# Optimization experiments

Hardware: AMD Instinct MI355X
Metric: run time of the kernel (lower is better)

## Reference

```python
import jax, jax.numpy as jnp
import numpy as np
from jax import lax

EPS = 1e-5
KH, KW, PAD, DIL = 3, 3, 1, 1


def _bilinear_gather(x, py, px):
    """x: [B,C,H,W]; py/px: [B,K,H,W] float sample coords. Returns [B,C,K,H,W].
    Zero-padding semantics (torchvision deform_conv2d): corners outside the image contribute 0."""
    B, C, H, W = x.shape
    K = py.shape[1]
    y0 = jnp.floor(py)
    x0 = jnp.floor(px)
    wy1 = py - y0
    wy0 = 1.0 - wy1
    wx1 = px - x0
    wx0 = 1.0 - wx1
    xf = x.reshape(B, C, H * W)

    def corner(yc, xc, w):
        valid = (yc >= 0) & (yc <= H - 1) & (xc >= 0) & (xc <= W - 1)
        yi = jnp.clip(yc, 0, H - 1).astype(jnp.int32)
        xi = jnp.clip(xc, 0, W - 1).astype(jnp.int32)
        lin = (yi * W + xi).reshape(B, -1)  # [B, K*H*W]
        v = jax.vmap(lambda xb, lb: xb[:, lb])(xf, lin)  # [B, C, K*H*W]
        return v * (w * valid.astype(x.dtype)).reshape(B, 1, -1)

    out = (corner(y0, x0, wy0 * wx0)
           + corner(y0, x0 + 1.0, wy0 * wx1)
           + corner(y0 + 1.0, x0, wy1 * wx0)
           + corner(y0 + 1.0, x0 + 1.0, wy1 * wx1))
    return out.reshape(B, C, K, H, W)


def _deform_conv(x, offset, w):
    B, C, H, W = x.shape
    K = KH * KW
    off = offset.reshape(B, K, 2, H, W)  # (dy, dx) per kernel tap
    ki = (jnp.arange(K) // KW - PAD).astype(x.dtype)  # kernel row offset (dil=1)
    kj = (jnp.arange(K) % KW - PAD).astype(x.dtype)
    hh = jnp.arange(H).astype(x.dtype)
    ww = jnp.arange(W).astype(x.dtype)
    py = hh[None, None, :, None] + ki[None, :, None, None] + off[:, :, 0]
    px = ww[None, None, None, :] + kj[None, :, None, None] + off[:, :, 1]
    val = _bilinear_gather(x, py, px)  # [B,C,K,H,W]
    return jnp.einsum('bckhw,ock->bohw', val, w.reshape(w.shape[0], C, K))


def _bn(x, gamma, beta, mean, var):
    inv = gamma * lax.rsqrt(var + EPS)
    return x * inv[None, :, None, None] + (beta - mean * inv)[None, :, None, None]


def setup_inputs() -> dict:
    key = jax.random.key(0)
    ks = jax.random.split(key, 12)
    B, C, H, W = 4, 128, 128, 128
    return {
        'x': jax.random.normal(ks[0], (B, C, H, W), jnp.float32),
        'offset': jax.random.normal(ks[1], (B, 2 * KH * KW, H, W), jnp.float32),
        'w1': jax.random.normal(ks[2], (C, C, KH, KW), jnp.float32) * 0.05,
        'bn1_gamma': jax.random.uniform(ks[3], (C,), jnp.float32, 0.5, 1.5),
        'bn1_beta': jax.random.normal(ks[4], (C,), jnp.float32) * 0.1,
        'bn1_mean': jax.random.normal(ks[5], (C,), jnp.float32) * 0.1,
        'bn1_var': jax.random.uniform(ks[6], (C,), jnp.float32, 0.5, 1.5),
        'w2': jax.random.normal(ks[7], (C, C, KH, KW), jnp.float32) * 0.05,
        'bn2_gamma': jax.random.uniform(ks[8], (C,), jnp.float32, 0.5, 1.5),
        'bn2_beta': jax.random.normal(ks[9], (C,), jnp.float32) * 0.1,
        'bn2_mean': jax.random.normal(ks[10], (C,), jnp.float32) * 0.1,
        'bn2_var': jax.random.uniform(ks[11], (C,), jnp.float32, 0.5, 1.5),
    }


def reference(x, offset, w1, bn1_gamma, bn1_beta, bn1_mean, bn1_var,
              w2, bn2_gamma, bn2_beta, bn2_mean, bn2_var):
    identity = x
    out = _deform_conv(x, offset, w1)
    out = jax.nn.relu(_bn(out, bn1_gamma, bn1_beta, bn1_mean, bn1_var))
    out = lax.conv_general_dilated(out, w2, window_strides=(1, 1),
                                   padding=((PAD, PAD), (PAD, PAD)),
                                   dimension_numbers=('NCHW', 'OIHW', 'NCHW'))
    out = _bn(out, bn2_gamma, bn2_beta, bn2_mean, bn2_var)
    out = jax.nn.relu(out + identity)
    return out
```

## Files before the change

kernel.cpp:

```cpp
#include <hip/hip_runtime.h>
#include <hip/hip_fp16.h>
#include <stdint.h>

#define B_ 4
#define C_ 128
#define H_ 128
#define W_ 128
#define HW 16384

typedef _Float16 h8 __attribute__((ext_vector_type(8)));
typedef float f32x16 __attribute__((ext_vector_type(16)));

__device__ __forceinline__ unsigned cvtpk_f16(float lo, float hi) {
    auto r = __builtin_amdgcn_cvt_pkrtz(lo, hi);
    return *(unsigned*)&r;
}

__device__ __forceinline__ unsigned blend_h2(unsigned c0, unsigned c1, unsigned c2, unsigned c3,
                                             __half2 G0, __half2 G1, __half2 G2, __half2 G3) {
    __half2 s = __hmul2(G0, *(__half2*)&c0);
    s = __hfma2(G1, *(__half2*)&c1, s);
    s = __hfma2(G2, *(__half2*)&c2, s);
    s = __hfma2(G3, *(__half2*)&c3, s);
    return *(unsigned*)&s;
}

__device__ __forceinline__ void gll16(const void* g, void* l) {
    __builtin_amdgcn_global_load_lds((const unsigned int*)g, (unsigned int*)l, 16, 0, 0);
}

__global__ __launch_bounds__(256) void prep_all(const float* __restrict__ x,
                                                unsigned short* __restrict__ xh,
                                                const float* __restrict__ w1,
                                                const float* __restrict__ w2,
                                                unsigned short* __restrict__ w1f,
                                                unsigned short* __restrict__ w2t,
                                                unsigned short* __restrict__ o1p,
                                                const float* g1, const float* b1, const float* m1, const float* v1,
                                                const float* g2, const float* b2, const float* m2, const float* v2,
                                                float* inv1, float* sh1, float* inv2, float* sh2) {
    __shared__ unsigned short tile[32][36];
    int blk = blockIdx.x;
    int tid = threadIdx.x;
    if (blk >= 1282) {
        int nb = blk - 1282;
        int wt = nb & 3, ct = (nb >> 2) & 3, h = (nb >> 4) & 127, b = nb >> 11;
        int c = tid >> 3, seg = tid & 7;
        const float* srcp = x + ((size_t)((b * 128 + ct * 32 + c) * 128 + h) * 128) + wt * 32 + seg * 4;
        float4 v = *(const float4*)srcp;
        uint2 pk;
        pk.x = cvtpk_f16(v.x, v.y);
        pk.y = cvtpk_f16(v.z, v.w);
        *(uint2*)&tile[c][seg * 4] = pk;
        __syncthreads();
        int w = tid >> 3, s2 = tid & 7;
        unsigned a0 = tile[s2 * 4 + 0][w];
        unsigned a1 = tile[s2 * 4 + 1][w];
        unsigned a2 = tile[s2 * 4 + 2][w];
        unsigned a3 = tile[s2 * 4 + 3][w];
        uint2 o;
        o.x = (a1 << 16) | a0;
        o.y = (a3 << 16) | a2;
        *(uint2*)(xh + ((size_t)((b * 128 + h) * 128 + wt * 32 + w) * 128) + ct * 32 + s2 * 4) = o;
        return;
    }
    if (blk < 1152) {
        int i = blk * 256 + tid;
        if (i < 147456) {
            int o = i / 1152, rem = i % 1152;
            int c = rem / 9, tap = rem % 9;
            _Float16 hv = (_Float16)w1[i];
            int s = o >> 5;
            int ks = c >> 4;
            int l = (o & 31) | (((c >> 3) & 1) << 5);
            int jj = c & 7;
            w1f[(((tap * 4 + s) * 8 + ks) * 64 + l) * 8 + jj] = *(unsigned short*)&hv;
        } else {
            int j = i - 147456;
            int o = j / 1152, rem = j % 1152;
            int c = rem / 9, tap = rem % 9;
            _Float16 hv = (_Float16)w2[j];
            w2t[o * 1152 + tap * 128 + c] = *(unsigned short*)&hv;
        }
    } else if (blk < 1281) {
        int i = (blk - 1152) * 256 + tid;
        if (i < 33024) {
            int chunk = i & 15;
            int pos = i >> 4;
            int b = pos / 516;
            int r = pos % 516;
            int row, col;
            if (r < 130)      { row = 0;   col = r; }
            else if (r < 260) { row = 129; col = r - 130; }
            else { int j = r - 260; row = 1 + (j >> 1); col = (j & 1) * 129; }
            uint4 z = {0u, 0u, 0u, 0u};
            *(uint4*)((char*)o1p + (size_t)((b * 130 + row) * 130 + col) * 256 + chunk * 16) = z;
        }
    } else {
        if (tid < 128) {
            float iv = g1[tid] * rsqrtf(v1[tid] + 1e-5f);
            inv1[tid] = iv; sh1[tid] = b1[tid] - m1[tid] * iv;
        } else {
            int u = tid - 128;
            float iv = g2[u] * rsqrtf(v2[u] + 1e-5f);
            inv2[u] = iv; sh2[u] = b2[u] - m2[u] * iv;
        }
    }
}

__global__ __launch_bounds__(512, 4) void gemm1_k(
    const unsigned short* __restrict__ xh,
    const float* __restrict__ off,
    const unsigned short* __restrict__ w1f,
    const float* __restrict__ inv1,
    const float* __restrict__ sh1,
    unsigned short* __restrict__ out1p) {
    __shared__ __align__(16) char ldsv[2][16384];

    int bid = blockIdx.x;
    int swz = ((bid & 7) << 7) | (bid >> 3);
    int half = swz & 1, h = (swz >> 1) & 127, b = swz >> 8;
    int w0 = half * 64;
    int tid = threadIdx.x;
    int bH = b * H_;
    const char* xb8 = (const char*)xh;

    if (tid < 256) {
        int prow = tid >> 4;
        int seg = tid & 15;
        int sb = seg * 16;

        float dy[4], dx[4];
        unsigned PX[4][4];
        float g[4][4];
        uint4 buf[2][4];

#define OFFLOAD(TT) do { \
    int dyB_ = ((b * 18 + 2 * (TT)) * H_ + h) * W_ + w0; \
    _Pragma("unroll") \
    for (int c_ = 0; c_ < 4; ++c_) { \
        int p_ = prow + c_ * 16; \
        dy[c_] = off[dyB_ + p_]; \
        dx[c_] = off[dyB_ + HW + p_]; \
    } \
} while (0)

#define COORD(TT) do { \
    int kh_ = (TT) / 3 - 1, kw_ = (TT) % 3 - 1; \
    _Pragma("unroll") \
    for (int c_ = 0; c_ < 4; ++c_) { \
        int p_ = prow + c_ * 16; \
        float py_ = (float)(h + kh_) + dy[c_]; \
        float px_ = (float)(w0 + p_ + kw_) + dx[c_]; \
        float y0f_ = floorf(py_), x0f_ = floorf(px_); \
        int y0_ = (int)y0f_, x0_ = (int)x0f_; \
        float wy1_ = py_ - y0f_, wx1_ = px_ - x0f_; \
        float wy0_ = 1.f - wy1_, wx0_ = 1.f - wx1_; \
        int y1_ = y0_ + 1, x1_ = x0_ + 1; \
        g[c_][0] = ((unsigned)y0_ < 128u && (unsigned)x0_ < 128u) ? wy0_ * wx0_ : 0.f; \
        g[c_][1] = ((unsigned)y0_ < 128u && (unsigned)x1_ < 128u) ? wy0_ * wx1_ : 0.f; \
        g[c_][2] = ((unsigned)y1_ < 128u && (unsigned)x0_ < 128u) ? wy1_ * wx0_ : 0.f; \
        g[c_][3] = ((unsigned)y1_ < 128u && (unsigned)x1_ < 128u) ? wy1_ * wx1_ : 0.f; \
        int y0c_ = min(max(y0_, 0), 127), y1c_ = min(max(y1_, 0), 127); \
        int x0c_ = min(max(x0_, 0), 127), x1c_ = min(max(x1_, 0), 127); \
        int r0_ = (bH + y0c_) * W_, r1_ = (bH + y1c_) * W_; \
        PX[c_][0] = (unsigned)((r0_ + x0c_) * 256) + sb; \
        PX[c_][1] = (unsigned)((r0_ + x1c_) * 256) + sb; \
        PX[c_][2] = (unsigned)((r1_ + x0c_) * 256) + sb; \
        PX[c_][3] = (unsigned)((r1_ + x1c_) * 256) + sb; \
    } \
} while (0)

#define ISSUE2(cA, cB) do { \
    _Pragma("unroll") \
    for (int k_ = 0; k_ < 4; ++k_) buf[0][k_] = *(const uint4*)(xb8 + PX[cA][k_]); \
    _Pragma("unroll") \
    for (int k_ = 0; k_ < 4; ++k_) buf[1][k_] = *(const uint4*)(xb8 + PX[cB][k_]); \
} while (0)

#define BLEND1(VP, CC, BI) do { \
    __half2 G0_ = __float2half2_rn(g[CC][0]); \
    __half2 G1_ = __float2half2_rn(g[CC][1]); \
    __half2 G2_ = __float2half2_rn(g[CC][2]); \
    __half2 G3_ = __float2half2_rn(g[CC][3]); \
    uint4 st_; \
    st_.x = blend_h2(buf[BI][0].x, buf[BI][1].x, buf[BI][2].x, buf[BI][3].x, G0_, G1_, G2_, G3_); \
    st_.y = blend_h2(buf[BI][0].y, buf[BI][1].y, buf[BI][2].y, buf[BI][3].y, G0_, G1_, G2_, G3_); \
    st_.z = blend_h2(buf[BI][0].z, buf[BI][1].z, buf[BI][2].z, buf[BI][3].z, G0_, G1_, G2_, G3_); \
    st_.w = blend_h2(buf[BI][0].w, buf[BI][1].w, buf[BI][2].w, buf[BI][3].w, G0_, G1_, G2_, G3_); \
    int row_ = prow + (CC) * 16; \
    *(uint4*)(&ldsv[VP][0] + row_ * 256 + ((seg ^ (row_ & 15)) << 4)) = st_; \
} while (0)

#define GATHER(VP) do { \
    ISSUE2(0, 1); \
    BLEND1(VP, 0, 0); BLEND1(VP, 1, 1); \
    ISSUE2(2, 3); \
    BLEND1(VP, 2, 0); BLEND1(VP, 3, 1); \
} while (0)

        OFFLOAD(0);
        COORD(0);
        GATHER(0);
        OFFLOAD(1);
        __syncthreads();
        for (int t = 0; t < 9; ++t) {
            if (t < 8) {
                COORD(t + 1);
                GATHER((t + 1) & 1);
                if (t < 7) OFFLOAD(t + 2);
            }
            __syncthreads();
        }
#undef OFFLOAD
#undef COORD
#undef ISSUE2
#undef BLEND1
#undef GATHER
    } else {
        int ctid = tid - 256;
        int lane = ctid & 63, wq = ctid >> 6;
        int lp = lane & 31, hi = lane >> 5;
        int lsw = lp & 15;
        int bRow0 = lp * 256;
        int bRow1 = (32 + lp) * 256;

        f32x16 acc0 = {};
        f32x16 acc1 = {};
        h8 wreg[2][8];

        {
            const unsigned short* wb = w1f + wq * 4096 + lane * 8;
            #pragma unroll
            for (int ks = 0; ks < 8; ++ks) wreg[0][ks] = *(const h8*)(wb + ks * 512);
        }
        __syncthreads();
        #pragma unroll
        for (int t = 0; t < 9; ++t) {
            if (t < 8) {
                const unsigned short* wb = w1f + ((t + 1) * 4 + wq) * 4096 + lane * 8;
                #pragma unroll
                for (int ks = 0; ks < 8; ++ks) wreg[(t + 1) & 1][ks] = *(const h8*)(wb + ks * 512);
            }
            const char* vcur = &ldsv[t & 1][0];
            #pragma unroll
            for (int ks = 0; ks < 8; ++ks) {
                int q0 = 2 * ks + hi;
                int sl = (q0 ^ lsw) << 4;
                h8 b0 = *(const h8*)(vcur + bRow0 + sl);
                h8 b1 = *(const h8*)(vcur + bRow1 + sl);
                h8 a = wreg[t & 1][ks];
                acc0 = __builtin_amdgcn_mfma_f32_32x32x16_f16(a, b0, acc0, 0, 0, 0);
                acc1 = __builtin_amdgcn_mfma_f32_32x32x16_f16(a, b1, acc1, 0, 0, 0);
            }
            __syncthreads();
        }

        #pragma unroll
        for (int j = 0; j < 2; ++j) {
            int p = w0 + j * 32 + lp;
            size_t rowbase = (size_t)((b * 130 + h + 1) * 130 + 1 + p) * 128;
            #pragma unroll
            for (int k = 0; k < 4; ++k) {
                int o0 = wq * 32 + k * 8 + hi * 4;
                float4 iv = *(const float4*)(inv1 + o0);
                float4 sv = *(const float4*)(sh1 + o0);
                float e0, e1, e2, e3;
                if (j == 0) {
                    e0 = acc0[4 * k + 0]; e1 = acc0[4 * k + 1];
                    e2 = acc0[4 * k + 2]; e3 = acc0[4 * k + 3];
                } else {
                    e0 = acc1[4 * k + 0]; e1 = acc1[4 * k + 1];
                    e2 = acc1[4 * k + 2]; e3 = acc1[4 * k + 3];
                }
                float v0 = fmaxf(fmaf(e0, iv.x, sv.x), 0.f);
                float v1 = fmaxf(fmaf(e1, iv.y, sv.y), 0.f);
                float v2 = fmaxf(fmaf(e2, iv.z, sv.z), 0.f);
                float v3 = fmaxf(fmaf(e3, iv.w, sv.w), 0.f);
                uint2 pk2;
                pk2.x = cvtpk_f16(v0, v1);
                pk2.y = cvtpk_f16(v2, v3);
                *(uint2*)(out1p + rowbase + o0) = pk2;
            }
        }
    }
}

__global__ __launch_bounds__(512, 4) void gemm2_k(
    const unsigned short* __restrict__ out1p,
    const unsigned short* __restrict__ w2t,
    const unsigned short* __restrict__ xh,
    const float* __restrict__ inv2,
    const float* __restrict__ sh2,
    float* __restrict__ outp) {
    __shared__ __align__(16) char ldsS[33280];
    __shared__ __align__(16) char ldsw[32768];

    int bid = blockIdx.x;
    int swz = ((bid & 7) << 6) | (bid >> 3);
    int h = swz & 127, b = swz >> 7;
    int tid = threadIdx.x, lane = tid & 63, wv = tid >> 6;
    int wo = wv >> 2, wp = wv & 3;
    int lp = lane & 31, hi = lane >> 5;

    f32x16 acc0 = {};
    f32x16 acc1 = {};

    int aRow0 = (wo * 64 + lp) * 256;
    int aRow1 = aRow0 + 32 * 256;
    int lsw = lp & 15;

    for (int kh = 0; kh < 3; ++kh) {
        __syncthreads();
        const char* srow = (const char*)out1p + (size_t)((b * 130 + h + kh) * 130) * 256;
        #pragma unroll
        for (int it = 0; it < 5; ++it) {
            int ci = it * 512 + tid;
            if (ci < 2080) {
                int r = ci >> 4, q = ci & 15;
                gll16(srow + r * 256 + ((q ^ (r & 15)) << 4), ldsS + ci * 16);
            }
        }
        for (int kw = 0; kw < 3; ++kw) {
            if (kw) __syncthreads();
            int tap = kh * 3 + kw;
            #pragma unroll
            for (int it = 0; it < 4; ++it) {
                int ci = it * 512 + tid;
                int o = ci >> 4, q = ci & 15;
                gll16((const char*)w2t + o * 2304 + tap * 256 + ((q ^ (o & 15)) << 4), ldsw + ci * 16);
            }
            __syncthreads();
            int pr = (wp * 32 + lp + kw) * 256;
            int prw = (wp * 32 + lp + kw) & 15;
            #pragma unroll
            for (int ks = 0; ks < 8; ++ks) {
                int q0 = 2 * ks + hi;
                h8 bb = *(const h8*)(ldsS + pr + ((q0 ^ prw) << 4));
                int sl = (q0 ^ lsw) << 4;
                h8 a0 = *(const h8*)(ldsw + aRow0 + sl);
                h8 a1 = *(const h8*)(ldsw + aRow1 + sl);
                acc0 = __builtin_amdgcn_mfma_f32_32x32x16_f16(a0, bb, acc0, 0, 0, 0);
                acc1 = __builtin_amdgcn_mfma_f32_32x32x16_f16(a1, bb, acc1, 0, 0, 0);
            }
        }
    }

    int p = wp * 32 + lp;
    const unsigned short* xrow = xh + (size_t)((b * 128 + h) * 128 + p) * 128;
    #pragma unroll
    for (int t = 0; t < 2; ++t) {
        #pragma unroll
        for (int k = 0; k < 4; ++k) {
            int o0 = wo * 64 + t * 32 + k * 8 + hi * 4;
            uint2 rx = *(const uint2*)(xrow + o0);
            __half2 hx0 = *(__half2*)&rx.x;
            __half2 hx1 = *(__half2*)&rx.y;
            float x0 = __low2float(hx0), x1 = __high2float(hx0);
            float x2 = __low2float(hx1), x3 = __high2float(hx1);
            float e0, e1, e2, e3;
            if (t == 0) {
                e0 = acc0[4 * k + 0]; e1 = acc0[4 * k + 1];
                e2 = acc0[4 * k + 2]; e3 = acc0[4 * k + 3];
            } else {
                e0 = acc1[4 * k + 0]; e1 = acc1[4 * k + 1];
                e2 = acc1[4 * k + 2]; e3 = acc1[4 * k + 3];
            }
            size_t idx = ((size_t)(b * C_ + o0) * H_ + h) * W_ + p;
            outp[idx]            = fmaxf(fmaf(e0, inv2[o0 + 0], sh2[o0 + 0]) + x0, 0.f);
            outp[idx + HW]       = fmaxf(fmaf(e1, inv2[o0 + 1], sh2[o0 + 1]) + x1, 0.f);
            outp[idx + 2 * HW]   = fmaxf(fmaf(e2, inv2[o0 + 2], sh2[o0 + 2]) + x2, 0.f);
            outp[idx + 3 * HW]   = fmaxf(fmaf(e3, inv2[o0 + 3], sh2[o0 + 3]) + x3, 0.f);
        }
    }
}

extern "C" void kernel_launch(void* const* d_in, const int* in_sizes, int n_in,
                              void* d_out, int out_size, void* d_ws, size_t ws_size,
                              hipStream_t stream) {
    const float* x   = (const float*)d_in[0];
    const float* off = (const float*)d_in[1];
    const float* w1  = (const float*)d_in[2];
    const float* g1  = (const float*)d_in[3];
    const float* b1  = (const float*)d_in[4];
    const float* m1  = (const float*)d_in[5];
    const float* v1  = (const float*)d_in[6];
    const float* w2  = (const float*)d_in[7];
    const float* g2  = (const float*)d_in[8];
    const float* b2  = (const float*)d_in[9];
    const float* m2  = (const float*)d_in[10];
    const float* v2  = (const float*)d_in[11];
    float* outp = (float*)d_out;

    char* ws = (char*)d_ws;
    unsigned short* w1f = (unsigned short*)(ws);
    unsigned short* w2t = (unsigned short*)(ws + 294912);
    float* inv1 = (float*)(ws + 589824);
    float* sh1  = (float*)(ws + 590336);
    float* inv2 = (float*)(ws + 590848);
    float* sh2  = (float*)(ws + 591360);
    unsigned short* xh  = (unsigned short*)(ws + 591872);
    unsigned short* o1p = (unsigned short*)(ws + 17369088);

    prep_all<<<9474, 256, 0, stream>>>(x, xh, w1, w2, w1f, w2t, o1p,
                                       g1, b1, m1, v1, g2, b2, m2, v2,
                                       inv1, sh1, inv2, sh2);
    gemm1_k<<<1024, 512, 0, stream>>>(xh, off, w1f, inv1, sh1, o1p);
    gemm2_k<<<512, 512, 0, stream>>>(o1p, w2t, xh, inv2, sh2, outp);
}
```

Measured before the change: 87.25 us.

## Keep conv2 weights in registers via fragment layout, drop LDS weight staging

The w2 weights are now prepacked into the same MFMA fragment layout as w1. gemm2 loads them straight from global memory into registers, double-buffered one tap ahead, instead of staging each tap through LDS behind extra barriers. The wave split also changes: each wave now covers 32 output channels by 64 pixels instead of 64 by 32, so one A fragment is reused across two B tiles. This removes the per-tap LDS weight fill and two of the three syncs per kh row, at the cost of more register pressure and uncoalesced-ish global weight loads from L2.

```diff
diff --git a/kernel.cpp b/kernel.cpp
--- a/kernel.cpp
+++ b/kernel.cpp
@@ -34,7 +34,7 @@
                                                 const float* __restrict__ w1,
                                                 const float* __restrict__ w2,
                                                 unsigned short* __restrict__ w1f,
-                                                unsigned short* __restrict__ w2t,
+                                                unsigned short* __restrict__ w2f,
                                                 unsigned short* __restrict__ o1p,
                                                 const float* g1, const float* b1, const float* m1, const float* v1,
                                                 const float* g2, const float* b2, const float* m2, const float* v2,
@@ -66,22 +66,18 @@
     }
     if (blk < 1152) {
         int i = blk * 256 + tid;
-        if (i < 147456) {
-            int o = i / 1152, rem = i % 1152;
-            int c = rem / 9, tap = rem % 9;
-            _Float16 hv = (_Float16)w1[i];
-            int s = o >> 5;
-            int ks = c >> 4;
-            int l = (o & 31) | (((c >> 3) & 1) << 5);
-            int jj = c & 7;
-            w1f[(((tap * 4 + s) * 8 + ks) * 64 + l) * 8 + jj] = *(unsigned short*)&hv;
-        } else {
-            int j = i - 147456;
-            int o = j / 1152, rem = j % 1152;
-            int c = rem / 9, tap = rem % 9;
-            _Float16 hv = (_Float16)w2[j];
-            w2t[o * 1152 + tap * 128 + c] = *(unsigned short*)&hv;
-        }
+        const float* src = w1;
+        unsigned short* dst = w1f;
+        int j = i;
+        if (i >= 147456) { j = i - 147456; src = w2; dst = w2f; }
+        int o = j / 1152, rem = j % 1152;
+        int c = rem / 9, tap = rem % 9;
+        _Float16 hv = (_Float16)src[j];
+        int s = o >> 5;
+        int ks = c >> 4;
+        int l = (o & 31) | (((c >> 3) & 1) << 5);
+        int jj = c & 7;
+        dst[(((tap * 4 + s) * 8 + ks) * 64 + l) * 8 + jj] = *(unsigned short*)&hv;
     } else if (blk < 1281) {
         int i = (blk - 1152) * 256 + tid;
         if (i < 33024) {
@@ -288,78 +284,79 @@
 
 __global__ __launch_bounds__(512, 4) void gemm2_k(
     const unsigned short* __restrict__ out1p,
-    const unsigned short* __restrict__ w2t,
+    const unsigned short* __restrict__ w2f,
     const unsigned short* __restrict__ xh,
     const float* __restrict__ inv2,
     const float* __restrict__ sh2,
     float* __restrict__ outp) {
     __shared__ __align__(16) char ldsS[33280];
-    __shared__ __align__(16) char ldsw[32768];
 
     int bid = blockIdx.x;
     int swz = ((bid & 7) << 6) | (bid >> 3);
     int h = swz & 127, b = swz >> 7;
     int tid = threadIdx.x, lane = tid & 63, wv = tid >> 6;
-    int wo = wv >> 2, wp = wv & 3;
+    int wq = wv >> 1, wp = wv & 1;
     int lp = lane & 31, hi = lane >> 5;
+    int lsw = lp & 15;
 
     f32x16 acc0 = {};
     f32x16 acc1 = {};
-
-    int aRow0 = (wo * 64 + lp) * 256;
-    int aRow1 = aRow0 + 32 * 256;
-    int lsw = lp & 15;
-
-    for (int kh = 0; kh < 3; ++kh) {
-        __syncthreads();
-        const char* srow = (const char*)out1p + (size_t)((b * 130 + h + kh) * 130) * 256;
+    h8 wreg[2][8];
+
+    {
+        const unsigned short* wb = w2f + wq * 4096 + lane * 8;
         #pragma unroll
-        for (int it = 0; it < 5; ++it) {
-            int ci = it * 512 + tid;
-            if (ci < 2080) {
-                int r = ci >> 4, q = ci & 15;
-                gll16(srow + r * 256 + ((q ^ (r & 15)) << 4), ldsS + ci * 16);
-            }
-        }
-        for (int kw = 0; kw < 3; ++kw) {
-            if (kw) __syncthreads();
-            int tap = kh * 3 + kw;
+        for (int ks = 0; ks < 8; ++ks) wreg[0][ks] = *(const h8*)(wb + ks * 512);
+    }
+
+    #pragma unroll
+    for (int t = 0; t < 9; ++t) {
+        int kh = t / 3, kw = t % 3;
+        if (kw == 0) {
+            __syncthreads();
+            const char* srow = (const char*)out1p + (size_t)((b * 130 + h + kh) * 130) * 256;
             #pragma unroll
-            for (int it = 0; it < 4; ++it) {
+            for (int it = 0; it < 5; ++it) {
                 int ci = it * 512 + tid;
-                int o = ci >> 4, q = ci & 15;
-                gll16((const char*)w2t + o * 2304 + tap * 256 + ((q ^ (o & 15)) << 4), ldsw + ci * 16);
+                if (ci < 2080) {
+                    int r = ci >> 4, q = ci & 15;
+                    gll16(srow + r * 256 + ((q ^ (r & 15)) << 4), ldsS + ci * 16);
+                }
             }
             __syncthreads();
-            int pr = (wp * 32 + lp + kw) * 256;
-            int prw = (wp * 32 + lp + kw) & 15;
+        }
+        if (t < 8) {
+            const unsigned short* wb = w2f + ((t + 1) * 4 + wq) * 4096 + lane * 8;
             #pragma unroll
-            for (int ks = 0; ks < 8; ++ks) {
-                int q0 = 2 * ks + hi;
-                h8 bb = *(const h8*)(ldsS + pr + ((q0 ^ prw) << 4));
-                int sl = (q0 ^ lsw) << 4;
-                h8 a0 = *(const h8*)(ldsw + aRow0 + sl);
-                h8 a1 = *(const h8*)(ldsw + aRow1 + sl);
-                acc0 = __builtin_amdgcn_mfma_f32_32x32x16_f16(a0, bb, acc0, 0, 0, 0);
-                acc1 = __builtin_amdgcn_mfma_f32_32x32x16_f16(a1, bb, acc1, 0, 0, 0);
-            }
-        }
-    }
-
-    int p = wp * 32 + lp;
-    const unsigned short* xrow = xh + (size_t)((b * 128 + h) * 128 + p) * 128;
+            for (int ks = 0; ks < 8; ++ks) wreg[(t + 1) & 1][ks] = *(const h8*)(wb + ks * 512);
+        }
+        #pragma unroll
+        for (int ks = 0; ks < 8; ++ks) {
+            int q0 = 2 * ks + hi;
+            int pr0 = wp * 64 + lp + kw;
+            int pr1 = pr0 + 32;
+            h8 b0 = *(const h8*)(ldsS + pr0 * 256 + ((q0 ^ (pr0 & 15)) << 4));
+            h8 b1 = *(const h8*)(ldsS + pr1 * 256 + ((q0 ^ (pr1 & 15)) << 4));
+            h8 a = wreg[t & 1][ks];
+            acc0 = __builtin_amdgcn_mfma_f32_32x32x16_f16(a, b0, acc0, 0, 0, 0);
+            acc1 = __builtin_amdgcn_mfma_f32_32x32x16_f16(a, b1, acc1, 0, 0, 0);
+        }
+    }
+
     #pragma unroll
-    for (int t = 0; t < 2; ++t) {
+    for (int j = 0; j < 2; ++j) {
+        int p = wp * 64 + j * 32 + lp;
+        const unsigned short* xrow = xh + (size_t)((b * 128 + h) * 128 + p) * 128;
         #pragma unroll
         for (int k = 0; k < 4; ++k) {
-            int o0 = wo * 64 + t * 32 + k * 8 + hi * 4;
+            int o0 = wq * 32 + k * 8 + hi * 4;
             uint2 rx = *(const uint2*)(xrow + o0);
             __half2 hx0 = *(__half2*)&rx.x;
             __half2 hx1 = *(__half2*)&rx.y;
             float x0 = __low2float(hx0), x1 = __high2float(hx0);
             float x2 = __low2float(hx1), x3 = __high2float(hx1);
             float e0, e1, e2, e3;
-            if (t == 0) {
+            if (j == 0) {
                 e0 = acc0[4 * k + 0]; e1 = acc0[4 * k + 1];
                 e2 = acc0[4 * k + 2]; e3 = acc0[4 * k + 3];
             } else {
@@ -394,7 +391,7 @@
 
     char* ws = (char*)d_ws;
     unsigned short* w1f = (unsigned short*)(ws);
-    unsigned short* w2t = (unsigned short*)(ws + 294912);
+    unsigned short* w2f = (unsigned short*)(ws + 294912);
     float* inv1 = (float*)(ws + 589824);
     float* sh1  = (float*)(ws + 590336);
     float* inv2 = (float*)(ws + 590848);
@@ -402,9 +399,9 @@
     unsigned short* xh  = (unsigned short*)(ws + 591872);
     unsigned short* o1p = (unsigned short*)(ws + 17369088);
 
-    prep_all<<<9474, 256, 0, stream>>>(x, xh, w1, w2, w1f, w2t, o1p,
+    prep_all<<<9474, 256, 0, stream>>>(x, xh, w1, w2, w1f, w2f, o1p,
                                        g1, b1, m1, v1, g2, b2, m2, v2,
                                        inv1, sh1, inv2, sh2);
     gemm1_k<<<1024, 512, 0, stream>>>(xh, off, w1f, inv1, sh1, o1p);
-    gemm2_k<<<512, 512, 0, stream>>>(o1p, w2t, xh, inv2, sh2, outp);
-}
+    gemm2_k<<<512, 512, 0, stream>>>(o1p, w2f, xh, inv2, sh2, outp);
+}
```

Result: no change. 86.67 us (-0.7%).
